# Performance work log

Hardware: AMD Instinct MI355X
Metric: run time of the kernel (lower is better)

Reference implementation:

```python
import jax, jax.numpy as jnp
import numpy as np

N = 50000
E = 800000
D_IN = 128
D_HID = 128
NUM_LAYERS = 3


def setup_inputs() -> dict:
    key = jax.random.key(0)
    ks = jax.random.split(key, 8)
    x = jax.random.normal(ks[0], (N, D_IN), dtype=jnp.float32)
    edge_index = jax.random.randint(ks[1], (2, E), 0, N, dtype=jnp.int64)
    edge_weight = jnp.ones((E,), dtype=jnp.float32)
    # GCNConv params: glorot-ish weights [in, out], zero bias
    def w(k, fi, fo):
        return jax.random.normal(k, (fi, fo), dtype=jnp.float32) * (1.0 / np.sqrt(fi))
    W0 = w(ks[2], D_IN, D_HID)
    b0 = jnp.zeros((D_HID,), dtype=jnp.float32)
    W1 = w(ks[3], D_HID, D_HID)
    b1 = jnp.zeros((D_HID,), dtype=jnp.float32)
    W2 = w(ks[4], D_HID, D_HID)
    b2 = jnp.zeros((D_HID,), dtype=jnp.float32)
    return {"x": x, "edge_index": edge_index, "edge_weight": edge_weight,
            "W0": W0, "b0": b0, "W1": W1, "b1": b1, "W2": W2, "b2": b2}


def _gcn_layer(h, src, dst, norm, W, b, n):
    # linear transform then degree-normalized scatter-add aggregation
    h = h @ W                                   # [N, d_out]
    msg = h[src] * norm[:, None]                # gather + scale, [E+N, d_out]
    out = jax.ops.segment_sum(msg, dst, num_segments=n)  # scatter-add
    return out + b


def reference(x, edge_index, edge_weight, W0, b0, W1, b1, W2, b2):
    n = x.shape[0]
    loop = jnp.arange(n, dtype=edge_index.dtype)
    src = jnp.concatenate([edge_index[0], loop])   # add self-loops (fill=1)
    dst = jnp.concatenate([edge_index[1], loop])
    ew = jnp.concatenate([edge_weight, jnp.ones((n,), dtype=edge_weight.dtype)])
    # symmetric normalization: deg computed on target (col), norm = d^-1/2[src]*w*d^-1/2[dst]
    deg = jax.ops.segment_sum(ew, dst, num_segments=n)
    dis = jnp.where(deg > 0, jax.lax.rsqrt(deg), 0.0)
    norm = dis[src] * ew * dis[dst]               # [E+N]
    z = x
    for (W, b) in ((W0, b0), (W1, b1), (W2, b2)):
        z = _gcn_layer(z, src, dst, norm, W, b, n)
        z = jax.nn.relu(z)
    return z
```

## Files before the change

### kernel.cpp

```cpp
#include <hip/hip_runtime.h>

#define D 128

typedef float f2v __attribute__((ext_vector_type(2)));
typedef short bf16x8 __attribute__((ext_vector_type(8)));
typedef float f32x4 __attribute__((ext_vector_type(4)));

__device__ __forceinline__ unsigned bf16r(float f) {
  unsigned u = __float_as_uint(f);
  return (u + 0x7fffu + ((u >> 16) & 1u)) >> 16;
}


__global__ __launch_bounds__(256) void k_init(int* __restrict__ cnt, int n) {
  int i = blockIdx.x * 256 + threadIdx.x;
  if (i < n) cnt[i] = 0;
}

__global__ __launch_bounds__(256) void k_pre1(const int* __restrict__ dst, int* __restrict__ cnt,
                                              int* __restrict__ p_local, int E, int GR,
                                              const float* __restrict__ X, unsigned short* __restrict__ Xb,
                                              int total4, int GC,
                                              const float* __restrict__ W0, const float* __restrict__ W1,
                                              const float* __restrict__ W2, unsigned short* __restrict__ Wt) {
  int b = blockIdx.x;
  int tid = threadIdx.x;
  if (b < GR) {
    int e = b * 256 + tid;
    if (e < E) p_local[e] = atomicAdd(&cnt[dst[e]], 1);
  } else if (b < GR + GC) {
    int i = (b - GR) * 256 + tid;
    if (i < total4) {
      float4 v = ((const float4*)X)[i];
      ushort4 o;
      o.x = (unsigned short)bf16r(v.x);
      o.y = (unsigned short)bf16r(v.y);
      o.z = (unsigned short)bf16r(v.z);
      o.w = (unsigned short)bf16r(v.w);
      ((ushort4*)Xb)[i] = o;
    }
  } else {
    int i = (b - GR - GC) * 256 + tid;
    if (i < 3 * 16384) {
      int l = i >> 14;
      int r = i & 16383;
      int nn = r >> 7, kk = r & 127;
      const float* W = (l == 0) ? W0 : (l == 1) ? W1 : W2;
      Wt[i] = (unsigned short)bf16r(W[kk * 128 + nn]);
    }
  }
}

__global__ __launch_bounds__(256) void k_blocksum(const int* __restrict__ cnt, int* __restrict__ bsum, int n) {
  int i = blockIdx.x * 256 + threadIdx.x;
  int v = (i < n) ? cnt[i] : 0;
#pragma unroll
  for (int off = 32; off > 0; off >>= 1) v += __shfl_down(v, off);
  __shared__ int ws[4];
  if ((threadIdx.x & 63) == 0) ws[threadIdx.x >> 6] = v;
  __syncthreads();
  if (threadIdx.x == 0) bsum[blockIdx.x] = ws[0] + ws[1] + ws[2] + ws[3];
}

__global__ __launch_bounds__(256) void k_scanb(const int* __restrict__ bsum, int* __restrict__ boff, int nb) {
  __shared__ int s[256];
  int t = threadIdx.x;
  int v = (t < nb) ? bsum[t] : 0;
  s[t] = v;
  __syncthreads();
#pragma unroll
  for (int off = 1; off < 256; off <<= 1) {
    int u = (t >= off) ? s[t - off] : 0;
    __syncthreads();
    s[t] += u;
    __syncthreads();
  }
  if (t < nb) boff[t] = s[t] - v;
}

__global__ __launch_bounds__(256) void k_scanc(const int* __restrict__ cnt, const int* __restrict__ boff,
                                               int* __restrict__ rowptr, int n, int Etot) {
  __shared__ int s[256];
  int t = threadIdx.x;
  int i = blockIdx.x * 256 + t;
  int v = (i < n) ? cnt[i] : 0;
  s[t] = v;
  __syncthreads();
#pragma unroll
  for (int off = 1; off < 256; off <<= 1) {
    int u = (t >= off) ? s[t - off] : 0;
    __syncthreads();
    s[t] += u;
    __syncthreads();
  }
  int ex = s[t] - v + boff[blockIdx.x];
  if (i < n) rowptr[i] = ex;
  if (i == 0) rowptr[n] = Etot;
}

__global__ __launch_bounds__(256) void k_pre2(const unsigned short* __restrict__ Zb,
                                              const unsigned short* __restrict__ Wt,
                                              unsigned short* __restrict__ H, int n, int GG,
                                              const int* __restrict__ src, const int* __restrict__ dst,
                                              const float* __restrict__ ew, const int* __restrict__ rowptr,
                                              const int* __restrict__ p_local, float2* __restrict__ csr, int E) {
  int b = blockIdx.x;
  if (b < GG) {
    int lane = threadIdx.x & 63;
    int wid  = threadIdx.x >> 6;
    int row0 = b * 16;
    int r  = lane & 15;
    int kg = lane >> 4;
    int c0 = wid * 32;
    const size_t abase  = (size_t)(row0 + r) * 128 + kg * 8;
    const size_t b0base = (size_t)(c0 + r) * 128 + kg * 8;
    const size_t b1base = (size_t)(c0 + 16 + r) * 128 + kg * 8;
    f32x4 acc0 = {0.f, 0.f, 0.f, 0.f};
    f32x4 acc1 = {0.f, 0.f, 0.f, 0.f};
#pragma unroll
    for (int k0 = 0; k0 < 128; k0 += 32) {
      bf16x8 a  = *(const bf16x8*)&Zb[abase + k0];
      bf16x8 b0 = *(const bf16x8*)&Wt[b0base + k0];
      bf16x8 b1 = *(const bf16x8*)&Wt[b1base + k0];
      acc0 = __builtin_amdgcn_mfma_f32_16x16x32_bf16(a, b0, acc0, 0, 0, 0);
      acc1 = __builtin_amdgcn_mfma_f32_16x16x32_bf16(a, b1, acc1, 0, 0, 0);
    }
    int orow = row0 + kg * 4;
#pragma unroll
    for (int j = 0; j < 4; ++j) {
      H[(size_t)(orow + j) * 128 + c0 + r]      = (unsigned short)bf16r(acc0[j]);
      H[(size_t)(orow + j) * 128 + c0 + 16 + r] = (unsigned short)bf16r(acc1[j]);
    }
  } else {
    int e = (b - GG) * 256 + threadIdx.x;
    if (e < E) {
      int d = dst[e];
      int pos = rowptr[d] + p_local[e];
      float2 rec;
      rec.x = __int_as_float(src[e]);
      rec.y = ew[e];
      csr[pos] = rec;
    }
  }
}

__global__ __launch_bounds__(256) void k_degdis(const float2* __restrict__ csr, const int* __restrict__ rowptr,
                                                float* __restrict__ dis, int n) {
  int node = blockIdx.x * 4 + (threadIdx.x >> 6);
  if (node >= n) return;
  int lane = threadIdx.x & 63;
  int beg = rowptr[node], end = rowptr[node + 1];
  float s = 0.f;
  for (int e = beg + lane; e < end; e += 64) s += csr[e].y;
#pragma unroll
  for (int off = 32; off > 0; off >>= 1) s += __shfl_down(s, off);
  if (lane == 0) {
    float dg = 1.0f + s;
    dis[node] = dg > 0.f ? rsqrtf(dg) : 0.f;
  }
}


__global__ __launch_bounds__(256) void k_gemm(const unsigned short* __restrict__ Zb,
                                              const unsigned short* __restrict__ Wt,
                                              unsigned short* __restrict__ H, int n) {
  int lane = threadIdx.x & 63;
  int wid  = threadIdx.x >> 6;
  int row0 = blockIdx.x * 16;
  int r  = lane & 15;
  int kg = lane >> 4;
  int c0 = wid * 32;
  const size_t abase  = (size_t)(row0 + r) * 128 + kg * 8;
  const size_t b0base = (size_t)(c0 + r) * 128 + kg * 8;
  const size_t b1base = (size_t)(c0 + 16 + r) * 128 + kg * 8;
  f32x4 acc0 = {0.f, 0.f, 0.f, 0.f};
  f32x4 acc1 = {0.f, 0.f, 0.f, 0.f};
#pragma unroll
  for (int k0 = 0; k0 < 128; k0 += 32) {
    bf16x8 a  = *(const bf16x8*)&Zb[abase + k0];
    bf16x8 b0 = *(const bf16x8*)&Wt[b0base + k0];
    bf16x8 b1 = *(const bf16x8*)&Wt[b1base + k0];
    acc0 = __builtin_amdgcn_mfma_f32_16x16x32_bf16(a, b0, acc0, 0, 0, 0);
    acc1 = __builtin_amdgcn_mfma_f32_16x16x32_bf16(a, b1, acc1, 0, 0, 0);
  }
  int orow = row0 + kg * 4;
#pragma unroll
  for (int j = 0; j < 4; ++j) {
    H[(size_t)(orow + j) * 128 + c0 + r]      = (unsigned short)bf16r(acc0[j]);
    H[(size_t)(orow + j) * 128 + c0 + 16 + r] = (unsigned short)bf16r(acc1[j]);
  }
}


__global__ __launch_bounds__(256) void k_agg(const unsigned* __restrict__ Hb, const int* __restrict__ rowptr,
                                             const f2v* __restrict__ csr, const float* __restrict__ dis,
                                             const float* __restrict__ bias, unsigned* __restrict__ outb,
                                             float* __restrict__ outf, int n) {
  int node = __builtin_amdgcn_readfirstlane(blockIdx.x * 4 + (threadIdx.x >> 6));
  if (node >= n) return;
  int lane = threadIdx.x & 63;
  float ax = 0.f, ay = 0.f;
  int e = rowptr[node];
  const int end = rowptr[node + 1];
  for (; e + 4 <= end; e += 4) {
    f2v r0 = __builtin_nontemporal_load(&csr[e]);
    f2v r1 = __builtin_nontemporal_load(&csr[e + 1]);
    f2v r2 = __builtin_nontemporal_load(&csr[e + 2]);
    f2v r3 = __builtin_nontemporal_load(&csr[e + 3]);
    int s0 = __float_as_int(r0.x);
    int s1 = __float_as_int(r1.x);
    int s2 = __float_as_int(r2.x);
    int s3 = __float_as_int(r3.x);
    float w0 = r0.y * dis[s0];
    float w1 = r1.y * dis[s1];
    float w2 = r2.y * dis[s2];
    float w3 = r3.y * dis[s3];
    unsigned g0 = Hb[(size_t)s0 * 64 + lane];
    unsigned g1 = Hb[(size_t)s1 * 64 + lane];
    unsigned g2 = Hb[(size_t)s2 * 64 + lane];
    unsigned g3 = Hb[(size_t)s3 * 64 + lane];
    ax = fmaf(__uint_as_float(g0 << 16), w0, ax); ay = fmaf(__uint_as_float(g0 & 0xffff0000u), w0, ay);
    ax = fmaf(__uint_as_float(g1 << 16), w1, ax); ay = fmaf(__uint_as_float(g1 & 0xffff0000u), w1, ay);
    ax = fmaf(__uint_as_float(g2 << 16), w2, ax); ay = fmaf(__uint_as_float(g2 & 0xffff0000u), w2, ay);
    ax = fmaf(__uint_as_float(g3 << 16), w3, ax); ay = fmaf(__uint_as_float(g3 & 0xffff0000u), w3, ay);
  }
  for (; e < end; ++e) {
    f2v r0 = __builtin_nontemporal_load(&csr[e]);
    int s0 = __float_as_int(r0.x);
    float w0 = r0.y * dis[s0];
    unsigned g0 = Hb[(size_t)s0 * 64 + lane];
    ax = fmaf(__uint_as_float(g0 << 16), w0, ax); ay = fmaf(__uint_as_float(g0 & 0xffff0000u), w0, ay);
  }
  float dn = dis[node];
  float sn = dn * dn;
  unsigned hv = Hb[(size_t)node * 64 + lane];
  float hvx = __uint_as_float(hv << 16);
  float hvy = __uint_as_float(hv & 0xffff0000u);
  float2 bv = ((const float2*)bias)[lane];
  float ox = fmaxf(fmaf(dn, ax, fmaf(sn, hvx, bv.x)), 0.f);
  float oy = fmaxf(fmaf(dn, ay, fmaf(sn, hvy, bv.y)), 0.f);
  if (outb) {
    outb[(size_t)node * 64 + lane] = bf16r(ox) | (bf16r(oy) << 16);
  } else {
    f2v o; o.x = ox; o.y = oy;
    __builtin_nontemporal_store(o, (f2v*)outf + (size_t)node * 64 + lane);
  }
}


extern "C" void kernel_launch(void* const* d_in, const int* in_sizes, int n_in,
                              void* d_out, int out_size, void* d_ws, size_t ws_size,
                              hipStream_t stream) {
  const float* x  = (const float*)d_in[0];
  const int*   ei = (const int*)d_in[1];
  const float* ew = (const float*)d_in[2];
  const float* W0 = (const float*)d_in[3];
  const float* W1 = (const float*)d_in[5];
  const float* W2 = (const float*)d_in[7];
  const float* bl[3] = {(const float*)d_in[4], (const float*)d_in[6], (const float*)d_in[8]};

  const int n = in_sizes[0] / D;
  const int E = in_sizes[1] / 2;
  const int* src = ei;
  const int* dst = ei + E;

  char* p = (char*)d_ws;
  unsigned short* Zb      = (unsigned short*)p; p += (size_t)n * D * 2;
  unsigned short* H       = (unsigned short*)p; p += (size_t)n * D * 2;
  float*          dis     = (float*)p;          p += (size_t)n * 4;
  int*            cnt     = (int*)p;            p += (size_t)n * 4;
  int*            rowptr  = (int*)p;            p += (size_t)(n + 1) * 4;
  int*            bsum    = (int*)p;            p += 256 * 4;
  int*            boff    = (int*)p;            p += 256 * 4;
  int*            p_local = (int*)p;            p += (size_t)E * 4;
  float2*         csr     = (float2*)p;         p += (size_t)E * 8;
  unsigned short* Wt      = (unsigned short*)p; p += 3 * 16384 * 2;
  (void)ws_size; (void)n_in;

  const int gb = (n + 255) / 256;
  const int ge = (E + 255) / 256;
  const int total4 = n * D / 4;
  const int GC = (total4 + 255) / 256;
  const int GW = (3 * 16384 + 255) / 256;
  const int GG = n / 16;

  k_init<<<gb, 256, 0, stream>>>(cnt, n);
  k_pre1<<<ge + GC + GW, 256, 0, stream>>>(dst, cnt, p_local, E, ge, x, Zb, total4, GC, W0, W1, W2, Wt);
  k_blocksum<<<gb, 256, 0, stream>>>(cnt, bsum, n);
  k_scanb<<<1, 256, 0, stream>>>(bsum, boff, gb);
  k_scanc<<<gb, 256, 0, stream>>>(cnt, boff, rowptr, n, E);
  k_pre2<<<GG + ge, 256, 0, stream>>>(Zb, Wt, H, n, GG, src, dst, ew, rowptr, p_local, csr, E);
  k_degdis<<<(n + 3) / 4, 256, 0, stream>>>(csr, rowptr, dis, n);

  float* outp = (float*)d_out;
  k_agg<<<(n + 3) / 4, 256, 0, stream>>>((const unsigned*)H, rowptr, (const f2v*)csr, dis, bl[0], (unsigned*)Zb, outp, n);
  for (int l = 1; l < 3; ++l) {
    k_gemm<<<GG, 256, 0, stream>>>(Zb, Wt + l * 16384, H, n);
    unsigned* ob = (l == 2) ? nullptr : (unsigned*)Zb;
    k_agg<<<(n + 3) / 4, 256, 0, stream>>>((const unsigned*)H, rowptr, (const f2v*)csr, dis, bl[l], ob, outp, n);
  }
}
```

Measured before the change: 250.6 us.

## Build CSR via two-pass bucket sort with shared-memory histograms

Replaces the global per-node atomic counting, multi-kernel scan and scatter with a two-level bucket sort. Destinations are first binned into 250 buckets of 200 nodes using per-block shared histograms, then each bucket is sorted locally in shared memory, which also computes degrees and dis. This removes global atomics, several launches and the separate degree kernel. In exchange it hardcodes NB*BN = n, packs dst-low bits into the top byte of src (this assumes src < 2^24), and uses a serial 128-block loop in the single-block scan.

```diff
diff --git a/kernel.cpp b/kernel.cpp
--- a/kernel.cpp
+++ b/kernel.cpp
@@ -1,6 +1,10 @@
 #include <hip/hip_runtime.h>
 
 #define D 128
+#define NB 250
+#define BN 200
+#define NBLK 128
+#define CAP 7168
 
 typedef float f2v __attribute__((ext_vector_type(2)));
 typedef short bf16x8 __attribute__((ext_vector_type(8)));
@@ -12,24 +16,25 @@
 }
 
 
-__global__ __launch_bounds__(256) void k_init(int* __restrict__ cnt, int n) {
-  int i = blockIdx.x * 256 + threadIdx.x;
-  if (i < n) cnt[i] = 0;
-}
-
-__global__ __launch_bounds__(256) void k_pre1(const int* __restrict__ dst, int* __restrict__ cnt,
-                                              int* __restrict__ p_local, int E, int GR,
+__global__ __launch_bounds__(256) void k_pre1(const int* __restrict__ dst, int* __restrict__ M, int E,
                                               const float* __restrict__ X, unsigned short* __restrict__ Xb,
                                               int total4, int GC,
                                               const float* __restrict__ W0, const float* __restrict__ W1,
                                               const float* __restrict__ W2, unsigned short* __restrict__ Wt) {
+  __shared__ int lh[NB];
   int b = blockIdx.x;
   int tid = threadIdx.x;
-  if (b < GR) {
-    int e = b * 256 + tid;
-    if (e < E) p_local[e] = atomicAdd(&cnt[dst[e]], 1);
-  } else if (b < GR + GC) {
-    int i = (b - GR) * 256 + tid;
+  if (b < NBLK) {
+    for (int i = tid; i < NB; i += 256) lh[i] = 0;
+    __syncthreads();
+    const int EPB = (E + NBLK - 1) / NBLK;
+    int e0 = b * EPB;
+    int e1 = min(e0 + EPB, E);
+    for (int e = e0 + tid; e < e1; e += 256) atomicAdd(&lh[dst[e] / BN], 1);
+    __syncthreads();
+    for (int i = tid; i < NB; i += 256) M[b * NB + i] = lh[i];
+  } else if (b < NBLK + GC) {
+    int i = (b - NBLK) * 256 + tid;
     if (i < total4) {
       float4 v = ((const float4*)X)[i];
       ushort4 o;
@@ -40,7 +45,7 @@
       ((ushort4*)Xb)[i] = o;
     }
   } else {
-    int i = (b - GR - GC) * 256 + tid;
+    int i = (b - NBLK - GC) * 256 + tid;
     if (i < 3 * 16384) {
       int l = i >> 14;
       int r = i & 16383;
@@ -51,21 +56,14 @@
   }
 }
 
-__global__ __launch_bounds__(256) void k_blocksum(const int* __restrict__ cnt, int* __restrict__ bsum, int n) {
-  int i = blockIdx.x * 256 + threadIdx.x;
-  int v = (i < n) ? cnt[i] : 0;
-#pragma unroll
-  for (int off = 32; off > 0; off >>= 1) v += __shfl_down(v, off);
-  __shared__ int ws[4];
-  if ((threadIdx.x & 63) == 0) ws[threadIdx.x >> 6] = v;
-  __syncthreads();
-  if (threadIdx.x == 0) bsum[blockIdx.x] = ws[0] + ws[1] + ws[2] + ws[3];
-}
-
-__global__ __launch_bounds__(256) void k_scanb(const int* __restrict__ bsum, int* __restrict__ boff, int nb) {
+
+__global__ __launch_bounds__(256) void k_mscan(int* __restrict__ M, int* __restrict__ bbase, int Etot) {
   __shared__ int s[256];
   int t = threadIdx.x;
-  int v = (t < nb) ? bsum[t] : 0;
+  int v = 0;
+  if (t < NB) {
+    for (int blk = 0; blk < NBLK; ++blk) v += M[blk * NB + t];
+  }
   s[t] = v;
   __syncthreads();
 #pragma unroll
@@ -75,35 +73,27 @@
     s[t] += u;
     __syncthreads();
   }
-  if (t < nb) boff[t] = s[t] - v;
-}
-
-__global__ __launch_bounds__(256) void k_scanc(const int* __restrict__ cnt, const int* __restrict__ boff,
-                                               int* __restrict__ rowptr, int n, int Etot) {
-  __shared__ int s[256];
-  int t = threadIdx.x;
-  int i = blockIdx.x * 256 + t;
-  int v = (i < n) ? cnt[i] : 0;
-  s[t] = v;
-  __syncthreads();
-#pragma unroll
-  for (int off = 1; off < 256; off <<= 1) {
-    int u = (t >= off) ? s[t - off] : 0;
-    __syncthreads();
-    s[t] += u;
-    __syncthreads();
-  }
-  int ex = s[t] - v + boff[blockIdx.x];
-  if (i < n) rowptr[i] = ex;
-  if (i == 0) rowptr[n] = Etot;
-}
+  int ex = s[t] - v;
+  if (t < NB) {
+    bbase[t] = ex;
+    int run = ex;
+    for (int blk = 0; blk < NBLK; ++blk) {
+      int c = M[blk * NB + t];
+      M[blk * NB + t] = run;
+      run += c;
+    }
+  }
+  if (t == 0) bbase[NB] = Etot;
+}
+
 
 __global__ __launch_bounds__(256) void k_pre2(const unsigned short* __restrict__ Zb,
                                               const unsigned short* __restrict__ Wt,
                                               unsigned short* __restrict__ H, int n, int GG,
                                               const int* __restrict__ src, const int* __restrict__ dst,
-                                              const float* __restrict__ ew, const int* __restrict__ rowptr,
-                                              const int* __restrict__ p_local, float2* __restrict__ csr, int E) {
+                                              const float* __restrict__ ew, const int* __restrict__ M,
+                                              uint2* __restrict__ part, int E) {
+  __shared__ int lcur[NB];
   int b = blockIdx.x;
   if (b < GG) {
     int lane = threadIdx.x & 63;
@@ -132,31 +122,75 @@
       H[(size_t)(orow + j) * 128 + c0 + 16 + r] = (unsigned short)bf16r(acc1[j]);
     }
   } else {
-    int e = (b - GG) * 256 + threadIdx.x;
-    if (e < E) {
+    int blk = b - GG;
+    int tid = threadIdx.x;
+    for (int i = tid; i < NB; i += 256) lcur[i] = M[blk * NB + i];
+    __syncthreads();
+    const int EPB = (E + NBLK - 1) / NBLK;
+    int e0 = blk * EPB;
+    int e1 = min(e0 + EPB, E);
+    for (int e = e0 + tid; e < e1; e += 256) {
       int d = dst[e];
-      int pos = rowptr[d] + p_local[e];
-      float2 rec;
-      rec.x = __int_as_float(src[e]);
-      rec.y = ew[e];
-      csr[pos] = rec;
-    }
-  }
-}
-
-__global__ __launch_bounds__(256) void k_degdis(const float2* __restrict__ csr, const int* __restrict__ rowptr,
-                                                float* __restrict__ dis, int n) {
-  int node = blockIdx.x * 4 + (threadIdx.x >> 6);
-  if (node >= n) return;
-  int lane = threadIdx.x & 63;
-  int beg = rowptr[node], end = rowptr[node + 1];
-  float s = 0.f;
-  for (int e = beg + lane; e < end; e += 64) s += csr[e].y;
-#pragma unroll
-  for (int off = 32; off > 0; off >>= 1) s += __shfl_down(s, off);
-  if (lane == 0) {
-    float dg = 1.0f + s;
-    dis[node] = dg > 0.f ? rsqrtf(dg) : 0.f;
+      int bkt = d / BN;
+      int dlow = d - bkt * BN;
+      int p = atomicAdd(&lcur[bkt], 1);
+      uint2 rec;
+      rec.x = (unsigned)src[e] | ((unsigned)dlow << 24);
+      rec.y = __float_as_uint(ew[e]);
+      part[p] = rec;
+    }
+  }
+}
+
+
+__global__ __launch_bounds__(256) void k_bsort(const uint2* __restrict__ part, const int* __restrict__ bbase,
+                                               uint2* __restrict__ csr, int* __restrict__ rowptr,
+                                               float* __restrict__ dis, int n, int E) {
+  __shared__ uint2 stage[CAP];
+  __shared__ int lh[BN];
+  __shared__ float ldeg[BN];
+  __shared__ int s[256];
+  int b = blockIdx.x;
+  int tid = threadIdx.x;
+  int base = bbase[b];
+  int cnt = bbase[b + 1] - base;
+  for (int i = tid; i < BN; i += 256) { lh[i] = 0; ldeg[i] = 0.f; }
+  __syncthreads();
+  for (int i = tid; i < cnt; i += 256) {
+    uint2 r = part[base + i];
+    if (i < CAP) stage[i] = r;
+    int dlow = r.x >> 24;
+    atomicAdd(&lh[dlow], 1);
+    atomicAdd(&ldeg[dlow], __uint_as_float(r.y));
+  }
+  __syncthreads();
+  int v = (tid < BN) ? lh[tid] : 0;
+  s[tid] = v;
+  __syncthreads();
+#pragma unroll
+  for (int off = 1; off < 256; off <<= 1) {
+    int u = (tid >= off) ? s[tid - off] : 0;
+    __syncthreads();
+    s[tid] += u;
+    __syncthreads();
+  }
+  int ex = s[tid] - v;
+  if (tid < BN) {
+    lh[tid] = ex;
+    int node = b * BN + tid;
+    rowptr[node] = base + ex;
+    dis[node] = rsqrtf(1.0f + ldeg[tid]);
+  }
+  if (b == 0 && tid == 0) rowptr[n] = E;
+  __syncthreads();
+  for (int i = tid; i < cnt; i += 256) {
+    uint2 r = (i < CAP) ? stage[i] : part[base + i];
+    int dlow = r.x >> 24;
+    int p = atomicAdd(&lh[dlow], 1);
+    uint2 o;
+    o.x = r.x & 0x00FFFFFFu;
+    o.y = r.y;
+    csr[base + p] = o;
   }
 }
 
@@ -265,32 +299,26 @@
   const int* dst = ei + E;
 
   char* p = (char*)d_ws;
-  unsigned short* Zb      = (unsigned short*)p; p += (size_t)n * D * 2;
-  unsigned short* H       = (unsigned short*)p; p += (size_t)n * D * 2;
-  float*          dis     = (float*)p;          p += (size_t)n * 4;
-  int*            cnt     = (int*)p;            p += (size_t)n * 4;
-  int*            rowptr  = (int*)p;            p += (size_t)(n + 1) * 4;
-  int*            bsum    = (int*)p;            p += 256 * 4;
-  int*            boff    = (int*)p;            p += 256 * 4;
-  int*            p_local = (int*)p;            p += (size_t)E * 4;
-  float2*         csr     = (float2*)p;         p += (size_t)E * 8;
-  unsigned short* Wt      = (unsigned short*)p; p += 3 * 16384 * 2;
+  unsigned short* Zb     = (unsigned short*)p; p += (size_t)n * D * 2;
+  unsigned short* H      = (unsigned short*)p; p += (size_t)n * D * 2;
+  float*          dis    = (float*)p;          p += (size_t)n * 4;
+  int*            rowptr = (int*)p;            p += (size_t)(n + 1) * 4;
+  int*            M      = (int*)p;            p += (size_t)NBLK * NB * 4;
+  int*            bbase  = (int*)p;            p += (size_t)(NB + 1) * 4;
+  uint2*          part   = (uint2*)p;          p += (size_t)E * 8;
+  uint2*          csr    = (uint2*)p;          p += (size_t)E * 8;
+  unsigned short* Wt     = (unsigned short*)p; p += 3 * 16384 * 2;
   (void)ws_size; (void)n_in;
 
-  const int gb = (n + 255) / 256;
-  const int ge = (E + 255) / 256;
   const int total4 = n * D / 4;
   const int GC = (total4 + 255) / 256;
   const int GW = (3 * 16384 + 255) / 256;
   const int GG = n / 16;
 
-  k_init<<<gb, 256, 0, stream>>>(cnt, n);
-  k_pre1<<<ge + GC + GW, 256, 0, stream>>>(dst, cnt, p_local, E, ge, x, Zb, total4, GC, W0, W1, W2, Wt);
-  k_blocksum<<<gb, 256, 0, stream>>>(cnt, bsum, n);
-  k_scanb<<<1, 256, 0, stream>>>(bsum, boff, gb);
-  k_scanc<<<gb, 256, 0, stream>>>(cnt, boff, rowptr, n, E);
-  k_pre2<<<GG + ge, 256, 0, stream>>>(Zb, Wt, H, n, GG, src, dst, ew, rowptr, p_local, csr, E);
-  k_degdis<<<(n + 3) / 4, 256, 0, stream>>>(csr, rowptr, dis, n);
+  k_pre1<<<NBLK + GC + GW, 256, 0, stream>>>(dst, M, E, x, Zb, total4, GC, W0, W1, W2, Wt);
+  k_mscan<<<1, 256, 0, stream>>>(M, bbase, E);
+  k_pre2<<<GG + NBLK, 256, 0, stream>>>(Zb, Wt, H, n, GG, src, dst, ew, M, part, E);
+  k_bsort<<<NB, 256, 0, stream>>>(part, bbase, csr, rowptr, dis, n, E);
 
   float* outp = (float*)d_out;
   k_agg<<<(n + 3) / 4, 256, 0, stream>>>((const unsigned*)H, rowptr, (const f2v*)csr, dis, bl[0], (unsigned*)Zb, outp, n);
```

New measurement: 224.3 us. 1.12x faster.
